# Kernel tuning notes

Measured on AMD Instinct MI355X. Metric: run time of the kernel, lower is better.

## Reference

```python
import jax, jax.numpy as jnp
import numpy as np

N_NODES = 50000
NEG_SLOPE = 0.2  # PyG GATConv default leaky_relu slope
EPS = 1e-16      # PyG softmax denominator epsilon


def gat_layer(x, src, dst, W, a_src, a_dst, b):
    # x: [N, F_in], W: [F_in, H, F_out], a_*: [H, F_out], b: [F_out]
    h = jnp.einsum('ni,iho->nho', x, W)                      # [N, H, O]
    alpha_src = jnp.sum(h * a_src, axis=-1)                  # [N, H]
    alpha_dst = jnp.sum(h * a_dst, axis=-1)                  # [N, H]
    e = jax.nn.leaky_relu(alpha_src[src] + alpha_dst[dst], NEG_SLOPE)  # [E, H]
    # segment softmax over incoming edges of each destination node
    m = jax.ops.segment_max(e, dst, num_segments=N_NODES)   # [N, H]
    ex = jnp.exp(e - m[dst])
    s = jax.ops.segment_sum(ex, dst, num_segments=N_NODES)  # [N, H]
    alpha = ex / (s[dst] + EPS)                              # [E, H]
    out = jax.ops.segment_sum(alpha[:, :, None] * h[src], dst, num_segments=N_NODES)  # [N, H, O]
    out = out.mean(axis=1) + b                               # concat=False -> mean over heads
    return jax.nn.relu(out)                                  # norm=Identity, dropout p=0 no-op


def setup_inputs() -> dict:
    key = jax.random.key(0)
    ks = jax.random.split(key, 12)
    d = 64
    H = 4
    E = 800000
    inp = {
        'x': jax.random.normal(ks[0], (N_NODES, d), dtype=jnp.float32),
        'edge_index': jax.random.randint(ks[1], (2, E), 0, N_NODES, dtype=jnp.int64),
        'edge_attr': jax.random.normal(ks[2], (E, 8), dtype=jnp.float32),
        'dropout_rate': 0,
    }
    sc = 1.0 / np.sqrt(d)
    for li, base in ((1, 3), (2, 7)):
        inp[f'W{li}'] = jax.random.normal(ks[base], (d, H, d), dtype=jnp.float32) * sc
        inp[f'a_src{li}'] = jax.random.normal(ks[base + 1], (H, d), dtype=jnp.float32) * sc
        inp[f'a_dst{li}'] = jax.random.normal(ks[base + 2], (H, d), dtype=jnp.float32) * sc
        inp[f'b{li}'] = jnp.zeros((d,), dtype=jnp.float32)
    return inp


def reference(x, edge_index, edge_attr, dropout_rate,
              W1, a_src1, a_dst1, b1, W2, a_src2, a_dst2, b2):
    # edge_attr unused: GATConv built without edge_dim has no lin_edge.
    src, dst = edge_index[0], edge_index[1]
    x = gat_layer(x, src, dst, W1, a_src1, a_dst1, b1)
    x = gat_layer(x, src, dst, W2, a_src2, a_dst2, b2)
    return x
```

## Files before the change

### kernel.cpp

```cpp
#include <hip/hip_runtime.h>
#include <hip/hip_bf16.h>
#include <math.h>

#define N_NODES 50000
#define NEG_SLOPE 0.2f
#define EPS_DEN 1e-16f

#define NBUCK 196
#define NBLK  512

typedef float f4v __attribute__((ext_vector_type(4)));

__global__ void __launch_bounds__(256) prep_k(
    const float* __restrict__ W, const float* __restrict__ aS,
    const float* __restrict__ aD, float* __restrict__ WaSD)
{
    int tid = threadIdx.x;
    int h = tid >> 6, i = tid & 63;
    const float* wrow = W + (size_t)i * 256 + h * 64;
    const float* as = aS + h * 64;
    const float* ad = aD + h * 64;
    float ws = 0.f, wd = 0.f;
    #pragma unroll 8
    for (int o = 0; o < 64; ++o) {
        float w = wrow[o];
        ws = fmaf(w, as[o], ws);
        wd = fmaf(w, ad[o], wd);
    }
    WaSD[i * 8 + h]     = ws;
    WaSD[i * 8 + 4 + h] = wd;
}

__global__ void __launch_bounds__(256) alpha_k(
    const float* __restrict__ x, const float* __restrict__ WaSD,
    float* __restrict__ asrc, float* __restrict__ adst, int N)
{
    __shared__ float Wl[512];
    int tid = threadIdx.x;
    Wl[tid]       = WaSD[tid];
    Wl[tid + 256] = WaSD[tid + 256];
    __syncthreads();

    int node = blockIdx.x * 64 + (tid >> 2);
    int q = tid & 3;
    if (node >= N) return;

    float pS[4] = {0.f, 0.f, 0.f, 0.f};
    float pD[4] = {0.f, 0.f, 0.f, 0.f};
    const float* xp = x + (size_t)node * 64 + q * 16;
    #pragma unroll
    for (int j = 0; j < 4; ++j) {
        float4 xv = *(const float4*)(xp + j * 4);
        float xr[4] = {xv.x, xv.y, xv.z, xv.w};
        #pragma unroll
        for (int u = 0; u < 4; ++u) {
            int i = q * 16 + j * 4 + u;
            float4 wS = *(const float4*)(Wl + i * 8);
            float4 wD = *(const float4*)(Wl + i * 8 + 4);
            pS[0] = fmaf(xr[u], wS.x, pS[0]); pS[1] = fmaf(xr[u], wS.y, pS[1]);
            pS[2] = fmaf(xr[u], wS.z, pS[2]); pS[3] = fmaf(xr[u], wS.w, pS[3]);
            pD[0] = fmaf(xr[u], wD.x, pD[0]); pD[1] = fmaf(xr[u], wD.y, pD[1]);
            pD[2] = fmaf(xr[u], wD.z, pD[2]); pD[3] = fmaf(xr[u], wD.w, pD[3]);
        }
    }
    #pragma unroll
    for (int off = 1; off <= 2; off <<= 1) {
        #pragma unroll
        for (int h = 0; h < 4; ++h) {
            pS[h] += __shfl_xor(pS[h], off);
            pD[h] += __shfl_xor(pD[h], off);
        }
    }
    if (q == 0) {
        *(float4*)(asrc + 4 * (size_t)node) = make_float4(pS[0], pS[1], pS[2], pS[3]);
        *(float4*)(adst + 4 * (size_t)node) = make_float4(pD[0], pD[1], pD[2], pD[3]);
    }
}

__global__ void __launch_bounds__(256) hist_bucket_k(
    const int* __restrict__ ei, int* __restrict__ bh, int E)
{
    __shared__ int lh[NBUCK];
    int tid = threadIdx.x;
    for (int b = tid; b < NBUCK; b += 256) lh[b] = 0;
    __syncthreads();

    const int ch = (E + NBLK - 1) / NBLK;
    const int e0 = blockIdx.x * ch;
    const int e1 = min(e0 + ch, E);
    for (int e = e0 + tid; e < e1; e += 256)
        atomicAdd(&lh[ei[E + e] >> 8], 1);
    __syncthreads();
    for (int b = tid; b < NBUCK; b += 256)
        bh[(size_t)b * NBLK + blockIdx.x] = lh[b];
}

__global__ void __launch_bounds__(64) bscan_k(
    const int* __restrict__ bh, int* __restrict__ boffL, int* __restrict__ btot)
{
    const int b = blockIdx.x;
    const int lane = threadIdx.x;
    int v[8];
    int base = b * NBLK;
    #pragma unroll
    for (int u = 0; u < 8; ++u) v[u] = bh[base + lane * 8 + u];
    int t = 0;
    #pragma unroll
    for (int u = 0; u < 8; ++u) t += v[u];
    int run = t;
    #pragma unroll
    for (int off = 1; off < 64; off <<= 1) {
        int u = __shfl_up(run, off);
        if (lane >= off) run += u;
    }
    int lane_base = run - t;
    #pragma unroll
    for (int u = 0; u < 8; ++u) {
        boffL[base + lane * 8 + u] = lane_base;
        lane_base += v[u];
    }
    if (lane == 63) btot[b] = run;
}

__global__ void __launch_bounds__(256) btot_k(
    const int* __restrict__ btot, int* __restrict__ bbase,
    int* __restrict__ row, int N, int E)
{
    __shared__ int sd[256];
    int tid = threadIdx.x;
    int v = (tid < NBUCK) ? btot[tid] : 0;
    sd[tid] = v;
    __syncthreads();
    for (int off = 1; off < 256; off <<= 1) {
        int t = (tid >= off) ? sd[tid - off] : 0;
        __syncthreads();
        sd[tid] += t;
        __syncthreads();
    }
    if (tid < NBUCK) bbase[tid] = sd[tid] - v;
    if (tid == 0) { bbase[NBUCK] = E; row[N] = E; }
}

__global__ void __launch_bounds__(256) bplace_k(
    const int* __restrict__ ei, const int* __restrict__ bbase,
    const int* __restrict__ boffL, unsigned int* __restrict__ stage, int E)
{
    __shared__ int cur[NBUCK];
    int tid = threadIdx.x;
    for (int b = tid; b < NBUCK; b += 256)
        cur[b] = bbase[b] + boffL[(size_t)b * NBLK + blockIdx.x];
    __syncthreads();

    const int ch = (E + NBLK - 1) / NBLK;
    const int e0 = blockIdx.x * ch;
    const int e1 = min(e0 + ch, E);
    for (int e = e0 + tid; e < e1; e += 256) {
        int s = ei[e];
        int d = ei[E + e];
        int pos = atomicAdd(&cur[d >> 8], 1);
        stage[pos] = (unsigned int)s | ((unsigned int)(d & 255) << 16);
    }
}

__global__ void __launch_bounds__(256) bscatter_k(
    const unsigned int* __restrict__ stage, const int* __restrict__ bbase,
    int* __restrict__ row, int* __restrict__ psrc, int N)
{
    __shared__ int cnt[256];
    __shared__ int sd[256];
    __shared__ int cur[256];
    const int b = blockIdx.x;
    const int tid = threadIdx.x;
    const int nb0 = b << 8;
    const int es = bbase[b], ee = bbase[b + 1];

    cnt[tid] = 0;
    __syncthreads();
    for (int idx = es + tid; idx < ee; idx += 256)
        atomicAdd(&cnt[(stage[idx] >> 16) & 255], 1);
    __syncthreads();

    int v = cnt[tid];
    sd[tid] = v;
    __syncthreads();
    for (int off = 1; off < 256; off <<= 1) {
        int t = (tid >= off) ? sd[tid - off] : 0;
        __syncthreads();
        sd[tid] += t;
        __syncthreads();
    }
    int r = es + sd[tid] - v;
    int node = nb0 + tid;
    if (node < N) row[node] = r;
    cur[tid] = r;
    __syncthreads();

    for (int idx = es + tid; idx < ee; idx += 256) {
        unsigned int w = stage[idx];
        int pos = atomicAdd(&cur[(w >> 16) & 255], 1);
        psrc[pos] = w & 0xFFFF;
    }
}

#define MAXDEG4 64
#define ZT_STRIDE 260
__global__ void __launch_bounds__(256) aggzw_k(
    const float* __restrict__ x, const float* __restrict__ asrc,
    const float* __restrict__ adst, const int* __restrict__ row,
    const int* __restrict__ psrc, const float* __restrict__ W,
    const float* __restrict__ bias, float* __restrict__ out, int N)
{
    __shared__ float smem[9360];
    float4* pL = (float4*)smem;
    int*    sI = (int*)(smem + 4160);
    float*  zt = smem + 5200;
    float*  Wc = smem;

    const int tid  = threadIdx.x;
    const int lane = tid & 63;
    const int li   = lane & 15;
    const int slot = tid >> 4;
    const int n = blockIdx.x * 16 + slot;
    const bool active = n < N;

    int rs = 0, deg = 0;
    float4 ad = make_float4(0.f, 0.f, 0.f, 0.f);
    if (active) {
        rs  = row[n];
        deg = row[n + 1] - rs;
        ad  = *(const float4*)(adst + 4 * (size_t)n);
    }

    float m0 = -INFINITY, m1 = -INFINITY, m2 = -INFINITY, m3 = -INFINITY;
    float s0 = 0.f, s1 = 0.f, s2 = 0.f, s3 = 0.f;
    float4 a0 = make_float4(0.f,0.f,0.f,0.f), a1 = a0, a2 = a0, a3 = a0;
    const float* xb = x + (size_t)li * 4;

    if (deg <= MAXDEG4) {
        for (int j = li; j < deg; j += 16) {
            int s = psrc[rs + j];
            sI[slot * 65 + j] = s;
            float4 a = *(const float4*)(asrc + 4 * (size_t)s);
            float e0 = a.x + ad.x; e0 = e0 > 0.f ? e0 : NEG_SLOPE * e0;
            float e1 = a.y + ad.y; e1 = e1 > 0.f ? e1 : NEG_SLOPE * e1;
            float e2 = a.z + ad.z; e2 = e2 > 0.f ? e2 : NEG_SLOPE * e2;
            float e3 = a.w + ad.w; e3 = e3 > 0.f ? e3 : NEG_SLOPE * e3;
            pL[slot * 65 + j] = make_float4(e0, e1, e2, e3);
            m0 = fmaxf(m0, e0); m1 = fmaxf(m1, e1);
            m2 = fmaxf(m2, e2); m3 = fmaxf(m3, e3);
        }
        #pragma unroll
        for (int off = 1; off < 16; off <<= 1) {
            m0 = fmaxf(m0, __shfl_xor(m0, off));
            m1 = fmaxf(m1, __shfl_xor(m1, off));
            m2 = fmaxf(m2, __shfl_xor(m2, off));
            m3 = fmaxf(m3, __shfl_xor(m3, off));
        }
        for (int j = li; j < deg; j += 16) {
            float4 e = pL[slot * 65 + j];
            float4 p = make_float4(__expf(e.x - m0), __expf(e.y - m1),
                                   __expf(e.z - m2), __expf(e.w - m3));
            pL[slot * 65 + j] = p;
            s0 += p.x; s1 += p.y; s2 += p.z; s3 += p.w;
        }
        #pragma unroll
        for (int off = 1; off < 16; off <<= 1) {
            s0 += __shfl_xor(s0, off);
            s1 += __shfl_xor(s1, off);
            s2 += __shfl_xor(s2, off);
            s3 += __shfl_xor(s3, off);
        }
        #pragma unroll 2
        for (int j = 0; j < deg; ++j) {
            int s = sI[slot * 65 + j];
            float4 p = pL[slot * 65 + j];
            float4 xv = *(const float4*)(xb + (size_t)s * 64);
            a0.x = fmaf(p.x, xv.x, a0.x); a0.y = fmaf(p.x, xv.y, a0.y);
            a0.z = fmaf(p.x, xv.z, a0.z); a0.w = fmaf(p.x, xv.w, a0.w);
            a1.x = fmaf(p.y, xv.x, a1.x); a1.y = fmaf(p.y, xv.y, a1.y);
            a1.z = fmaf(p.y, xv.z, a1.z); a1.w = fmaf(p.y, xv.w, a1.w);
            a2.x = fmaf(p.z, xv.x, a2.x); a2.y = fmaf(p.z, xv.y, a2.y);
            a2.z = fmaf(p.z, xv.z, a2.z); a2.w = fmaf(p.z, xv.w, a2.w);
            a3.x = fmaf(p.w, xv.x, a3.x); a3.y = fmaf(p.w, xv.y, a3.y);
            a3.z = fmaf(p.w, xv.z, a3.z); a3.w = fmaf(p.w, xv.w, a3.w);
        }
    } else {
        for (int j = li; j < deg; j += 16) {
            int s = psrc[rs + j];
            float4 a = *(const float4*)(asrc + 4 * (size_t)s);
            float e0 = a.x + ad.x; e0 = e0 > 0.f ? e0 : NEG_SLOPE * e0;
            float e1 = a.y + ad.y; e1 = e1 > 0.f ? e1 : NEG_SLOPE * e1;
            float e2 = a.z + ad.z; e2 = e2 > 0.f ? e2 : NEG_SLOPE * e2;
            float e3 = a.w + ad.w; e3 = e3 > 0.f ? e3 : NEG_SLOPE * e3;
            m0 = fmaxf(m0, e0); m1 = fmaxf(m1, e1);
            m2 = fmaxf(m2, e2); m3 = fmaxf(m3, e3);
        }
        #pragma unroll
        for (int off = 1; off < 16; off <<= 1) {
            m0 = fmaxf(m0, __shfl_xor(m0, off));
            m1 = fmaxf(m1, __shfl_xor(m1, off));
            m2 = fmaxf(m2, __shfl_xor(m2, off));
            m3 = fmaxf(m3, __shfl_xor(m3, off));
        }
        for (int j = li; j < deg; j += 16) {
            int s = psrc[rs + j];
            float4 a = *(const float4*)(asrc + 4 * (size_t)s);
            float e0 = a.x + ad.x; e0 = e0 > 0.f ? e0 : NEG_SLOPE * e0;
            float e1 = a.y + ad.y; e1 = e1 > 0.f ? e1 : NEG_SLOPE * e1;
            float e2 = a.z + ad.z; e2 = e2 > 0.f ? e2 : NEG_SLOPE * e2;
            float e3 = a.w + ad.w; e3 = e3 > 0.f ? e3 : NEG_SLOPE * e3;
            s0 += __expf(e0 - m0); s1 += __expf(e1 - m1);
            s2 += __expf(e2 - m2); s3 += __expf(e3 - m3);
        }
        #pragma unroll
        for (int off = 1; off < 16; off <<= 1) {
            s0 += __shfl_xor(s0, off);
            s1 += __shfl_xor(s1, off);
            s2 += __shfl_xor(s2, off);
            s3 += __shfl_xor(s3, off);
        }
        for (int j = 0; j < deg; ++j) {
            int s = psrc[rs + j];
            float4 a = *(const float4*)(asrc + 4 * (size_t)s);
            float e0 = a.x + ad.x; e0 = e0 > 0.f ? e0 : NEG_SLOPE * e0;
            float e1 = a.y + ad.y; e1 = e1 > 0.f ? e1 : NEG_SLOPE * e1;
            float e2 = a.z + ad.z; e2 = e2 > 0.f ? e2 : NEG_SLOPE * e2;
            float e3 = a.w + ad.w; e3 = e3 > 0.f ? e3 : NEG_SLOPE * e3;
            float p0 = __expf(e0 - m0), p1 = __expf(e1 - m1);
            float p2 = __expf(e2 - m2), p3 = __expf(e3 - m3);
            float4 xv = *(const float4*)(xb + (size_t)s * 64);
            a0.x = fmaf(p0, xv.x, a0.x); a0.y = fmaf(p0, xv.y, a0.y);
            a0.z = fmaf(p0, xv.z, a0.z); a0.w = fmaf(p0, xv.w, a0.w);
            a1.x = fmaf(p1, xv.x, a1.x); a1.y = fmaf(p1, xv.y, a1.y);
            a1.z = fmaf(p1, xv.z, a1.z); a1.w = fmaf(p1, xv.w, a1.w);
            a2.x = fmaf(p2, xv.x, a2.x); a2.y = fmaf(p2, xv.y, a2.y);
            a2.z = fmaf(p2, xv.z, a2.z); a2.w = fmaf(p2, xv.w, a2.w);
            a3.x = fmaf(p3, xv.x, a3.x); a3.y = fmaf(p3, xv.y, a3.y);
            a3.z = fmaf(p3, xv.z, a3.z); a3.w = fmaf(p3, xv.w, a3.w);
        }
    }

    {
        float i0 = 0.25f / (s0 + EPS_DEN), i1 = 0.25f / (s1 + EPS_DEN);
        float i2 = 0.25f / (s2 + EPS_DEN), i3 = 0.25f / (s3 + EPS_DEN);
        float* zp = zt + slot * ZT_STRIDE + li * 4;
        *(float4*)(zp)       = make_float4(a0.x*i0, a0.y*i0, a0.z*i0, a0.w*i0);
        *(float4*)(zp + 64)  = make_float4(a1.x*i1, a1.y*i1, a1.z*i1, a1.w*i1);
        *(float4*)(zp + 128) = make_float4(a2.x*i2, a2.y*i2, a2.z*i2, a2.w*i2);
        *(float4*)(zp + 192) = make_float4(a3.x*i3, a3.y*i3, a3.z*i3, a3.w*i3);
    }

    const int og = tid & 15;
    const int nl = tid >> 4;
    float acc[4] = {0.f, 0.f, 0.f, 0.f};

    for (int cc = 0; cc < 4; ++cc) {
        __syncthreads();
        #pragma unroll
        for (int it = 0; it < 4; ++it) {
            int idx = tid + 256 * it;
            int k   = idx >> 4;
            int o4  = (idx & 15) << 2;
            *(float4*)(Wc + k * 64 + o4) =
                *(const float4*)(W + (size_t)k * 256 + cc * 64 + o4);
        }
        __syncthreads();

        const float* zrow = zt + nl * ZT_STRIDE + cc * 64;
        #pragma unroll
        for (int k4 = 0; k4 < 16; ++k4) {
            float4 zq = *(const float4*)(zrow + k4 * 4);
            float zr[4] = {zq.x, zq.y, zq.z, zq.w};
            #pragma unroll
            for (int u = 0; u < 4; ++u) {
                float4 wv = *(const float4*)(Wc + (k4 * 4 + u) * 64 + og * 4);
                acc[0] = fmaf(zr[u], wv.x, acc[0]);
                acc[1] = fmaf(zr[u], wv.y, acc[1]);
                acc[2] = fmaf(zr[u], wv.z, acc[2]);
                acc[3] = fmaf(zr[u], wv.w, acc[3]);
            }
        }
    }

    int gn = blockIdx.x * 16 + nl;
    if (gn < N) {
        float4 b4 = *(const float4*)(bias + og * 4);
        float4 o;
        o.x = fmaxf(acc[0] + b4.x, 0.f);
        o.y = fmaxf(acc[1] + b4.y, 0.f);
        o.z = fmaxf(acc[2] + b4.z, 0.f);
        o.w = fmaxf(acc[3] + b4.w, 0.f);
        *(float4*)(out + (size_t)gn * 64 + og * 4) = o;
    }
}

extern "C" void kernel_launch(void* const* d_in, const int* in_sizes, int n_in,
                              void* d_out, int out_size, void* d_ws, size_t ws_size,
                              hipStream_t stream)
{
    const float* x   = (const float*)d_in[0];
    const int*   ei  = (const int*)d_in[1];
    const float* W1  = (const float*)d_in[4];
    const float* as1 = (const float*)d_in[5];
    const float* ad1 = (const float*)d_in[6];
    const float* b1  = (const float*)d_in[7];
    const float* W2  = (const float*)d_in[8];
    const float* as2 = (const float*)d_in[9];
    const float* ad2 = (const float*)d_in[10];
    const float* b2  = (const float*)d_in[11];

    const int E = in_sizes[1] / 2;
    const int N = N_NODES;

    char* ws = (char*)d_ws;
    size_t off = 0;
    auto alloc = [&](size_t bytes) -> void* {
        void* p = ws + off;
        off = (off + bytes + 255) & ~(size_t)255;
        return p;
    };
    float*        x1    = (float*)alloc((size_t)N * 64 * 4);
    float*        asrc  = (float*)alloc((size_t)N * 4 * 4);
    float*        adst  = (float*)alloc((size_t)N * 4 * 4);
    float*        WaSD  = (float*)alloc(64 * 8 * 4);
    int*          row   = (int*)alloc((size_t)(N + 1) * 4);
    int*          psrc  = (int*)alloc((size_t)E * 4);
    int*          bh    = (int*)alloc((size_t)NBUCK * NBLK * 4);
    int*          boffL = (int*)alloc((size_t)NBUCK * NBLK * 4);
    int*          btot  = (int*)alloc((NBUCK + 1) * 4);
    int*          bbase = (int*)alloc((NBUCK + 1) * 4);
    unsigned int* stage = (unsigned int*)alloc((size_t)E * 4);

    hist_bucket_k<<<NBLK, 256, 0, stream>>>(ei, bh, E);
    bscan_k<<<NBUCK, 64, 0, stream>>>(bh, boffL, btot);
    btot_k<<<1, 256, 0, stream>>>(btot, bbase, row, N, E);
    bplace_k<<<NBLK, 256, 0, stream>>>(ei, bbase, boffL, stage, E);
    bscatter_k<<<NBUCK, 256, 0, stream>>>(stage, bbase, row, psrc, N);

    const int nblk64 = (N + 63) / 64;
    const int nblk16 = (N + 15) / 16;

    prep_k<<<1, 256, 0, stream>>>(W1, as1, ad1, WaSD);
    alpha_k<<<nblk64, 256, 0, stream>>>(x, WaSD, asrc, adst, N);
    aggzw_k<<<nblk16, 256, 0, stream>>>(x, asrc, adst, row, psrc, W1, b1, x1, N);

    prep_k<<<1, 256, 0, stream>>>(W2, as2, ad2, WaSD);
    alpha_k<<<nblk64, 256, 0, stream>>>(x1, WaSD, asrc, adst, N);
    aggzw_k<<<nblk16, 256, 0, stream>>>(x1, asrc, adst, row, psrc, W2, b2, (float*)d_out, N);
}
```

Baseline: 184.8 us.

## Register-block the fused z·W matmul with a split-K LDS reduction

Reorganizes the small per-block matmul of the aggregated features (16 nodes × 256) by W. The z tile is now stored transposed in LDS with a padded stride, and each thread computes a 4×4 register tile over a quarter of the K dimension. A final LDS reduction across the four K-slices then applies bias and ReLU. The aim is fewer LDS loads per FMA, since the old code had one float4 W load per four FMAs. In exchange it needs more LDS, an extra barrier and the reduction pass, and the transposed scalar stores into zt may cause bank conflicts.

```diff
diff --git a/kernel.cpp b/kernel.cpp
--- a/kernel.cpp
+++ b/kernel.cpp
@@ -203,18 +203,18 @@
 }
 
 #define MAXDEG4 64
-#define ZT_STRIDE 260
 __global__ void __launch_bounds__(256) aggzw_k(
     const float* __restrict__ x, const float* __restrict__ asrc,
     const float* __restrict__ adst, const int* __restrict__ row,
     const int* __restrict__ psrc, const float* __restrict__ W,
     const float* __restrict__ bias, float* __restrict__ out, int N)
 {
-    __shared__ float smem[9360];
+    __shared__ float smem[9808];
     float4* pL = (float4*)smem;
     int*    sI = (int*)(smem + 4160);
     float*  zt = smem + 5200;
     float*  Wc = smem;
+    float*  red = smem;
 
     const int tid  = threadIdx.x;
     const int lane = tid & 63;
@@ -340,19 +340,30 @@
         }
     }
 
-    {
+    if (active) {
         float i0 = 0.25f / (s0 + EPS_DEN), i1 = 0.25f / (s1 + EPS_DEN);
         float i2 = 0.25f / (s2 + EPS_DEN), i3 = 0.25f / (s3 + EPS_DEN);
-        float* zp = zt + slot * ZT_STRIDE + li * 4;
-        *(float4*)(zp)       = make_float4(a0.x*i0, a0.y*i0, a0.z*i0, a0.w*i0);
-        *(float4*)(zp + 64)  = make_float4(a1.x*i1, a1.y*i1, a1.z*i1, a1.w*i1);
-        *(float4*)(zp + 128) = make_float4(a2.x*i2, a2.y*i2, a2.z*i2, a2.w*i2);
-        *(float4*)(zp + 192) = make_float4(a3.x*i3, a3.y*i3, a3.z*i3, a3.w*i3);
-    }
-
+        float vh[4][4] = {
+            {a0.x * i0, a0.y * i0, a0.z * i0, a0.w * i0},
+            {a1.x * i1, a1.y * i1, a1.z * i1, a1.w * i1},
+            {a2.x * i2, a2.y * i2, a2.z * i2, a2.w * i2},
+            {a3.x * i3, a3.y * i3, a3.z * i3, a3.w * i3}
+        };
+        #pragma unroll
+        for (int h = 0; h < 4; ++h)
+            #pragma unroll
+            for (int u = 0; u < 4; ++u)
+                zt[(h * 64 + li * 4 + u) * 18 + slot] = vh[h][u];
+    }
+
+    const int ks = tid >> 6;
+    const int ng = (tid >> 4) & 3;
     const int og = tid & 15;
-    const int nl = tid >> 4;
-    float acc[4] = {0.f, 0.f, 0.f, 0.f};
+    float acc[4][4];
+    #pragma unroll
+    for (int i = 0; i < 4; ++i)
+        #pragma unroll
+        for (int j = 0; j < 4; ++j) acc[i][j] = 0.f;
 
     for (int cc = 0; cc < 4; ++cc) {
         __syncthreads();
@@ -366,31 +377,48 @@
         }
         __syncthreads();
 
-        const float* zrow = zt + nl * ZT_STRIDE + cc * 64;
-        #pragma unroll
-        for (int k4 = 0; k4 < 16; ++k4) {
-            float4 zq = *(const float4*)(zrow + k4 * 4);
-            float zr[4] = {zq.x, zq.y, zq.z, zq.w};
+        #pragma unroll
+        for (int kk = 0; kk < 16; ++kk) {
+            int kl = ks * 16 + kk;
+            int kg = cc * 64 + kl;
+            float2 zA = *(const float2*)(zt + kg * 18 + ng * 4);
+            float2 zB = *(const float2*)(zt + kg * 18 + ng * 4 + 2);
+            float4 wv = *(const float4*)(Wc + kl * 64 + og * 4);
+            float zr[4] = {zA.x, zA.y, zB.x, zB.y};
+            float wc4[4] = {wv.x, wv.y, wv.z, wv.w};
             #pragma unroll
-            for (int u = 0; u < 4; ++u) {
-                float4 wv = *(const float4*)(Wc + (k4 * 4 + u) * 64 + og * 4);
-                acc[0] = fmaf(zr[u], wv.x, acc[0]);
-                acc[1] = fmaf(zr[u], wv.y, acc[1]);
-                acc[2] = fmaf(zr[u], wv.z, acc[2]);
-                acc[3] = fmaf(zr[u], wv.w, acc[3]);
-            }
-        }
-    }
-
-    int gn = blockIdx.x * 16 + nl;
-    if (gn < N) {
-        float4 b4 = *(const float4*)(bias + og * 4);
-        float4 o;
-        o.x = fmaxf(acc[0] + b4.x, 0.f);
-        o.y = fmaxf(acc[1] + b4.y, 0.f);
-        o.z = fmaxf(acc[2] + b4.z, 0.f);
-        o.w = fmaxf(acc[3] + b4.w, 0.f);
-        *(float4*)(out + (size_t)gn * 64 + og * 4) = o;
+            for (int i = 0; i < 4; ++i)
+                #pragma unroll
+                for (int j = 0; j < 4; ++j)
+                    acc[i][j] = fmaf(zr[i], wc4[j], acc[i][j]);
+        }
+    }
+
+    __syncthreads();
+    #pragma unroll
+    for (int i = 0; i < 4; ++i)
+        *(float4*)(red + ((ks * 16 + ng * 4 + i) * 16 + og) * 4) =
+            make_float4(acc[i][0], acc[i][1], acc[i][2], acc[i][3]);
+    __syncthreads();
+
+    {
+        int nl = tid >> 4;
+        int o  = tid & 15;
+        const float4* r4 = (const float4*)red;
+        float4 p0 = r4[      nl * 16 + o];
+        float4 p1 = r4[256 + nl * 16 + o];
+        float4 p2 = r4[512 + nl * 16 + o];
+        float4 p3 = r4[768 + nl * 16 + o];
+        int gn = blockIdx.x * 16 + nl;
+        if (gn < N) {
+            float4 b4 = *(const float4*)(bias + o * 4);
+            float4 ov;
+            ov.x = fmaxf(p0.x + p1.x + p2.x + p3.x + b4.x, 0.f);
+            ov.y = fmaxf(p0.y + p1.y + p2.y + p3.y + b4.y, 0.f);
+            ov.z = fmaxf(p0.z + p1.z + p2.z + p3.z + b4.z, 0.f);
+            ov.w = fmaxf(p0.w + p1.w + p2.w + p3.w + b4.w, 0.f);
+            *(float4*)(out + (size_t)gn * 64 + o * 4) = ov;
+        }
     }
 }
 
```

Result: slower. 190.2 us (+2.9%).
